# Optimization experiments

Measured on AMD Instinct MI355X. Metric: run time of the kernel, lower is better.

The kernel has to match this reference:

```python
import jax, jax.numpy as jnp
import numpy as np

B, L, D, N, NL = 8, 32768, 64, 16, 4


def setup_inputs() -> dict:
    key = jax.random.key(0)
    ks = jax.random.split(key, 32)
    r = lambda i, shape, s=1.0: s * jax.random.normal(ks[i], shape, dtype=jnp.float32)
    return {
        "inputs": r(0, (B, L)),
        "w_init": r(1, (D, 1), 0.5), "b_init": r(2, (D,), 0.1),
        "s4_ln_w": 1.0 + r(3, (NL, D), 0.05), "s4_ln_b": r(4, (NL, D), 0.05),
        "log_dt": r(5, (NL, D), 0.5) - 4.0,          # dt ~ exp(-4) ~ 0.018
        "log_A_real": r(6, (NL, D, N), 0.3),
        "A_imag": r(7, (NL, D, N)),
        "C_re": r(8, (NL, D, N), 0.5), "C_im": r(9, (NL, D, N), 0.5),
        "D_skip": r(10, (NL, D)),
        "s4_out_w": r(11, (NL, 2 * D, D), 0.1), "s4_out_b": r(12, (NL, 2 * D), 0.05),
        "ff_ln_w": 1.0 + r(13, (NL, D), 0.05), "ff_ln_b": r(14, (NL, D), 0.05),
        "ff_w1": r(15, (NL, 2 * D, D), 0.1), "ff_b1": r(16, (NL, 2 * D), 0.05),
        "ff_w2": r(17, (NL, D, 2 * D), 0.1), "ff_b2": r(18, (NL, D), 0.05),
        "norm_w": 1.0 + r(19, (D,), 0.05), "norm_b": r(20, (D,), 0.05),
        "w_final1": r(21, (D, D), 0.1), "b_final1": r(22, (D,), 0.05),
        "w_zero": r(23, (1, D), 0.02), "b_zero": r(24, (1,), 0.01),
    }


def _ln(x, w, b):
    # layernorm over channel dim of [B, D, L] (TransposedLN)
    m = jnp.mean(x, axis=1, keepdims=True)
    v = jnp.var(x, axis=1, keepdims=True)
    return (x - m) * jax.lax.rsqrt(v + 1e-5) * w[None, :, None] + b[None, :, None]


def _s4d(z, log_dt, log_A_real, A_imag, C_re, C_im, D_skip):
    # S4D (diagonal SSM) with ZOH discretization; z: [B, D, L]
    Lq = z.shape[-1]
    dt = jnp.exp(log_dt)                              # [D]
    A = -jnp.exp(log_A_real) + 1j * A_imag            # [D, N]
    dtA = A * dt[:, None]                             # [D, N]
    C = (C_re + 1j * C_im) * (jnp.exp(dtA) - 1.0) / A # dC = C * (e^{dtA}-1)/A
    t = jnp.arange(Lq)
    # Vandermonde kernel K[d, l] = 2 Re sum_n dC[d,n] e^{dtA[d,n] * l}
    K = 2.0 * jnp.real(jnp.einsum('dn,dnl->dl', C, jnp.exp(dtA[:, :, None] * t)))
    n = 2 * Lq
    y = jnp.fft.irfft(jnp.fft.rfft(z, n) * jnp.fft.rfft(K, n)[None], n)[..., :Lq]
    return y + D_skip[None, :, None] * z


def reference(inputs, w_init, b_init, s4_ln_w, s4_ln_b, log_dt, log_A_real,
              A_imag, C_re, C_im, D_skip, s4_out_w, s4_out_b, ff_ln_w, ff_ln_b,
              ff_w1, ff_b1, ff_w2, ff_b2, norm_w, norm_b, w_final1, b_final1,
              w_zero, b_zero):
    # init conv (1x1) + ReLU; inputs [B, L] -> x [B, D, L]
    x = jax.nn.relu(jnp.einsum('dc,bcl->bdl', w_init, inputs[:, None, :])
                    + b_init[None, :, None])
    for i in range(NL):
        # --- S4 residual block: LN -> S4D -> GELU -> 1x1 conv to 2D -> GLU ---
        z = _ln(x, s4_ln_w[i], s4_ln_b[i])
        y = _s4d(z, log_dt[i], log_A_real[i], A_imag[i], C_re[i], C_im[i], D_skip[i])
        y = jax.nn.gelu(y)
        u = jnp.einsum('ed,bdl->bel', s4_out_w[i], y) + s4_out_b[i][None, :, None]
        a, g = jnp.split(u, 2, axis=1)
        x = x + a * jax.nn.sigmoid(g)
        z = _ln(x, ff_ln_w[i], ff_ln_b[i])
        h = jax.nn.gelu(jnp.einsum('ed,bdl->bel', ff_w1[i], z) + ff_b1[i][None, :, None])
        x = x + jnp.einsum('de,bel->bdl', ff_w2[i], h) + ff_b2[i][None, :, None]
    # final norm + conv head
    x = _ln(x, norm_w, norm_b)
    x = jax.nn.relu(jnp.einsum('ed,bdl->bel', w_final1, x) + b_final1[None, :, None])
    x = jnp.einsum('od,bdl->bol', w_zero, x) + b_zero[None, :, None]
    return x[:, 0, :]  # squeeze out_channels=1 -> [B, L]
```

## Files before the change

### kernel.cpp

```cpp
#include <hip/hip_runtime.h>
#include <cmath>

constexpr int Bq = 8, Lq = 32768, Dq = 64, Nq = 16, NLq = 4;
constexpr int CLq = 128, NCq = 256;
constexpr int PT = Bq * Lq / 16;

typedef _Float16 f16;
typedef _Float16 half2t __attribute__((ext_vector_type(2)));
typedef _Float16 half4 __attribute__((ext_vector_type(4)));
typedef _Float16 half8 __attribute__((ext_vector_type(8)));
typedef float f32x4 __attribute__((ext_vector_type(4)));
typedef float f32x2 __attribute__((ext_vector_type(2)));

static __device__ __forceinline__ float sigm(float x) { return 1.0f / (1.0f + __expf(-x)); }
static __device__ __forceinline__ float gelu_t(float x) {
  return x * sigm(1.5957691216057308f * fmaf(0.044715f * x * x, x, x));
}

__global__ __launch_bounds__(128) void k_wtall(
    const float* __restrict__ log_dt, const float* __restrict__ log_A_real,
    const float* __restrict__ A_imag, const float* __restrict__ C_re,
    const float* __restrict__ C_im, const float* __restrict__ dskip,
    f32x2* __restrict__ LCL, half8* __restrict__ TF, half8* __restrict__ VF,
    half8* __restrict__ WF) {
  __shared__ f32x2 pw[129][16];
  __shared__ f32x2 lamS[16], dcS[16];
  __shared__ float Ks[128];
  int d = blockIdx.x & 63, L = blockIdx.x >> 6;
  half8* TFl = TF + (size_t)L * 131072;
  half8* VFl = VF + (size_t)L * 32768;
  half8* WFl = WF + (size_t)L * 32768;
  int t = threadIdx.x;
  if (t < 16) {
    int di = L * 64 + d;
    int idx = di * 16 + t;
    float dt = expf(log_dt[di]);
    float Ar = -expf(log_A_real[idx]);
    float Ai = A_imag[idx];
    float dr = Ar * dt, dmi = Ai * dt;
    float er = expf(dr);
    float lr = er * cosf(dmi), li = er * sinf(dmi);
    float inv = 1.0f / (Ar * Ar + Ai * Ai);
    float e1r = lr - 1.0f, e1i = li;
    float qr = (e1r * Ar + e1i * Ai) * inv;
    float qi = (e1i * Ar - e1r * Ai) * inv;
    float cr = C_re[idx], ci = C_im[idx];
    lamS[t] = f32x2{lr, li};
    dcS[t] = f32x2{2.0f * (cr * qr - ci * qi), 2.0f * (cr * qi + ci * qr)};
    float erc = expf(dr * 128.0f);
    f32x2 l128 = f32x2{erc * cosf(dmi * 128.0f), erc * sinf(dmi * 128.0f)};
    pw[128][t] = l128;
    LCL[(size_t)L * 1024 + d * 16 + t] = l128;
  }
  __syncthreads();
#pragma unroll
  for (int n = 0; n < 16; n++) {
    f32x2 lam = lamS[n];
    float pr = 1.f, pi = 0.f, br = lam.x, bi = lam.y;
    int e = t;
    while (e) {
      if (e & 1) { float tt = pr * br - pi * bi; pi = fmaf(pr, bi, pi * br); pr = tt; }
      float t2 = br * br - bi * bi; bi = 2.f * br * bi; br = t2; e >>= 1;
    }
    pw[t][n] = f32x2{pr, pi};
  }
  __syncthreads();
  {
    float k = 0.f;
#pragma unroll
    for (int n = 0; n < 16; n++) {
      f32x2 dc = dcS[n];
      f32x2 p = pw[t][n];
      k += dc.x * p.x - dc.y * p.y;
    }
    if (t == 0) k += dskip[L * 64 + d];
    Ks[t] = k;
  }
  __syncthreads();
  for (int s = t; s < 2048; s += 128) {
    int ln = s & 63, kt = (s >> 6) & 3, mt = s >> 8;
    int jo = mt * 16 + (ln & 15);
    int ji0 = kt * 32 + (ln >> 4) * 8;
    half8 v;
#pragma unroll
    for (int jj = 0; jj < 8; jj++) {
      int ji = ji0 + jj;
      v[jj] = (jo >= ji) ? (f16)Ks[jo - ji] : (f16)0.f;
    }
    TFl[(size_t)d * 2048 + s] = v;
  }
  for (int s = t; s < 512; s += 128) {
    int ln = s & 63, mt = s >> 6;
    int jo = mt * 16 + (ln & 15);
    int q0 = (ln >> 4) * 8;
    half8 v;
#pragma unroll
    for (int jj = 0; jj < 8; jj++) {
      int q = q0 + jj, n = q >> 1;
      f32x2 dc = dcS[n];
      f32x2 p = pw[jo + 1][n];
      float wr = dc.x * p.x - dc.y * p.y;
      float wi = dc.x * p.y + dc.y * p.x;
      v[jj] = (q & 1) ? (f16)(-wi) : (f16)wr;
    }
    VFl[(size_t)d * 512 + s] = v;
  }
  for (int s = t; s < 512; s += 128) {
    int ln = s & 63, kt = (s >> 6) & 3, nt = s >> 8;
    int p_ = nt * 16 + (ln & 15);
    int n = p_ >> 1;
    int j0 = kt * 32 + (ln >> 4) * 8;
    half8 v;
#pragma unroll
    for (int jj = 0; jj < 8; jj++) {
      f32x2 p = pw[127 - (j0 + jj)][n];
      v[jj] = (p_ & 1) ? (f16)p.y : (f16)p.x;
    }
    WFl[(size_t)d * 512 + s] = v;
  }
}

__global__ __launch_bounds__(512) void k_init3(
    const float* __restrict__ inp, const float* __restrict__ w_init,
    const float* __restrict__ b_init, const float* __restrict__ lnw,
    const float* __restrict__ lnb, float* __restrict__ X, f16* __restrict__ Z16) {
  __shared__ __align__(16) f16 ztile[64 * 132];
  int tid = threadIdx.x;
  int widx = tid >> 6, lane = tid & 63;
  int pl = lane & 15, qh = lane >> 4;
  for (int k = 0; k < 4; ++k) {
    int pt = blockIdx.x * 8 + widx + k * 4096;
    int pos = pt * 16 + pl;
    float v = inp[pos];
    float s = 0.f, s2 = 0.f;
    f32x4 o[4];
#pragma unroll
    for (int q = 0; q < 4; q++) {
      int d0 = q * 16 + qh * 4;
      f32x4 w4 = *(const f32x4*)(w_init + d0);
      f32x4 b4 = *(const f32x4*)(b_init + d0);
#pragma unroll
      for (int j = 0; j < 4; j++) {
        float t = fmaf(w4[j], v, b4[j]);
        t = t > 0.f ? t : 0.f;
        o[q][j] = t; s += t; s2 += t * t;
      }
      *(f32x4*)(X + (size_t)pos * 64 + d0) = o[q];
    }
    s += __shfl_xor(s, 16); s += __shfl_xor(s, 32);
    s2 += __shfl_xor(s2, 16); s2 += __shfl_xor(s2, 32);
    float m = s * (1.0f / 64.0f);
    float rstd = rsqrtf(s2 * (1.0f / 64.0f) - m * m + 1e-5f);
    int prow = widx * 16 + pl;
#pragma unroll
    for (int q = 0; q < 4; q++) {
      int d0 = q * 16 + qh * 4;
      f32x4 lw = *(const f32x4*)(lnw + d0);
      f32x4 lb = *(const f32x4*)(lnb + d0);
#pragma unroll
      for (int r = 0; r < 4; r++)
        ztile[(d0 + r) * 132 + prow] = (f16)fmaf((o[q][r] - m) * rstd, lw[r], lb[r]);
    }
    __syncthreads();
    {
      int d = tid >> 3, c0 = (tid & 7) * 16;
      half8 z0 = *(const half8*)(ztile + d * 132 + c0);
      half8 z1 = *(const half8*)(ztile + d * 132 + c0 + 8);
      size_t zoff = (size_t)d * 262144 + (size_t)(blockIdx.x * 8 + k * 4096) * 16;
      *(half8*)(Z16 + zoff + c0) = z0;
      *(half8*)(Z16 + zoff + c0 + 8) = z1;
    }
    __syncthreads();
  }
}

__global__ __launch_bounds__(256) void k_p1g(
    const f16* __restrict__ Z16, const half8* __restrict__ WF, f16* __restrict__ S16) {
  int tid = threadIdx.x;
  int lane = tid & 63;
  int task = blockIdx.x * 4 + (tid >> 6);
  int d = task >> 7, bct = task & 127;
  int bc0 = bct * 16;
  int pl = lane & 15, qh = lane >> 4;
  half8 az[4];
  const f16* zp = Z16 + ((size_t)d * 2048 + bc0 + pl) * 128 + qh * 8;
#pragma unroll
  for (int kt = 0; kt < 4; kt++) az[kt] = *(const half8*)(zp + kt * 32);
#pragma unroll
  for (int nt = 0; nt < 2; nt++) {
    f32x4 acc = f32x4{0.f, 0.f, 0.f, 0.f};
#pragma unroll
    for (int kt = 0; kt < 4; kt++)
      acc = __builtin_amdgcn_mfma_f32_16x16x32_f16(az[kt], WF[(size_t)d * 512 + (nt * 4 + kt) * 64 + lane], acc, 0, 0, 0);
#pragma unroll
    for (int r = 0; r < 4; r++)
      S16[((size_t)d * 2048 + bc0 + qh * 4 + r) * 32 + nt * 16 + pl] = (f16)acc[r];
  }
}

__global__ __launch_bounds__(128) void k_pass2(
    const f16* __restrict__ S16, const f32x2* __restrict__ LCLl, f16* __restrict__ Sc) {
  int d = blockIdx.x;
  int t = threadIdx.x;
  int n = t & 15, b = t >> 4;
  f32x2 lam = LCLl[d * 16 + n];
  float cr = 0.f, ci = 0.f;
  size_t base = ((size_t)d * 2048 + b * 256) * 32 + 2 * n;
  const f16* sp = S16 + base;
  f16* cp = Sc + base;
#pragma unroll 8
  for (int c = 0; c < 256; c++) {
    *(half2t*)(cp + (size_t)c * 32) = half2t{(f16)cr, (f16)ci};
    half2t v = *(const half2t*)(sp + (size_t)c * 32);
    float nr = fmaf(lam.x, cr, fmaf(-lam.y, ci, (float)v[0]));
    float ni = fmaf(lam.x, ci, fmaf(lam.y, cr, (float)v[1]));
    cr = nr; ci = ni;
  }
}

__global__ __launch_bounds__(256) void k_p3g2(
    const f16* __restrict__ Z16, const f16* __restrict__ Sc,
    const half8* __restrict__ TF, const half8* __restrict__ VF,
    f16* __restrict__ Y16) {
  int tid = threadIdx.x;
  int lane = tid & 63, widx = tid >> 6;
  int bct = blockIdx.x & 127, dg = blockIdx.x >> 7;
  int bc0 = bct * 16;
  int dbase = dg * 16 + widx * 4;
  int pl = lane & 15, qh = lane >> 4;
  half8 zb[4][4];
  half8 sb[4];
#pragma unroll
  for (int di = 0; di < 4; di++) {
    int d = dbase + di;
    const f16* zp = Z16 + ((size_t)d * 2048 + bc0 + pl) * 128 + qh * 8;
#pragma unroll
    for (int kt = 0; kt < 4; kt++) zb[di][kt] = *(const half8*)(zp + kt * 32);
    sb[di] = *(const half8*)(Sc + ((size_t)d * 2048 + bc0 + pl) * 32 + qh * 8);
  }
#pragma unroll
  for (int mt = 0; mt < 8; mt++) {
    const int KTM = mt / 2 + 1;
    f32x4 acc[4];
#pragma unroll
    for (int di = 0; di < 4; di++) {
      int d = dbase + di;
      acc[di] = f32x4{0.f, 0.f, 0.f, 0.f};
      const half8* tfp = TF + ((size_t)d * 8 + mt) * 256 + lane;
#pragma unroll
      for (int kt = 0; kt < KTM; kt++)
        acc[di] = __builtin_amdgcn_mfma_f32_16x16x32_f16(tfp[kt * 64], zb[di][kt], acc[di], 0, 0, 0);
      acc[di] = __builtin_amdgcn_mfma_f32_16x16x32_f16(VF[((size_t)d * 8 + mt) * 64 + lane], sb[di], acc[di], 0, 0, 0);
    }
#pragma unroll
    for (int r = 0; r < 4; r++) {
      int pos = (bc0 + pl) * 128 + mt * 16 + qh * 4 + r;
      half4 pk = half4{(f16)gelu_t(acc[0][r]), (f16)gelu_t(acc[1][r]),
                       (f16)gelu_t(acc[2][r]), (f16)gelu_t(acc[3][r])};
      *(half4*)(Y16 + (size_t)pos * 64 + dbase) = pk;
    }
  }
}

template <int WZ>
__global__ __launch_bounds__(512) void k_gluff3(
    const f16* __restrict__ Y16, const float* __restrict__ Wg, const float* __restrict__ bg,
    const float* __restrict__ W1, const float* __restrict__ b1,
    const float* __restrict__ W2, const float* __restrict__ b2,
    const float* __restrict__ lnw, const float* __restrict__ lnb,
    const float* __restrict__ nlnw, const float* __restrict__ nlnb,
    float* __restrict__ X, f16* __restrict__ Z16,
    const float* __restrict__ Wf, const float* __restrict__ bfb,
    const float* __restrict__ wz, const float* __restrict__ bz,
    float* __restrict__ outp) {
  __shared__ __align__(16) char smem[68352];
  int tid = threadIdx.x;
#pragma unroll
  for (int it = 0; it < 2; it++) {
    int s = it * 512 + tid;
    int l = s & 63, ks = (s >> 6) & 1, et = s >> 7;
    const float* wp = Wg + (et * 16 + (l & 15)) * 64 + ks * 32 + (l >> 4) * 8;
    f32x4 w0 = *(const f32x4*)wp, w1 = *(const f32x4*)(wp + 4);
    *(half8*)(smem + s * 16) = half8{(f16)w0[0], (f16)w0[1], (f16)w0[2], (f16)w0[3],
                                     (f16)w1[0], (f16)w1[1], (f16)w1[2], (f16)w1[3]};
  }
#pragma unroll
  for (int it = 0; it < 2; it++) {
    int s = it * 512 + tid;
    int l = s & 63, ks = (s >> 6) & 1, et = s >> 7;
    int pls = l & 15, qhs = l >> 4;
    const float* wp = W1 + (et * 16 + pls) * 64 + ks * 32 + qhs * 4;
    f32x4 w0 = *(const f32x4*)wp;
    f32x4 w1 = *(const f32x4*)(wp + 16);
    *(half8*)(smem + 16384 + s * 16) = half8{(f16)w0[0], (f16)w0[1], (f16)w0[2], (f16)w0[3],
                                             (f16)w1[0], (f16)w1[1], (f16)w1[2], (f16)w1[3]};
  }
#pragma unroll
  for (int it = 0; it < 2; it++) {
    int s = it * 512 + tid;
    int l = s & 63, ks = (s >> 6) & 3, dt = s >> 8;
    int pls = l & 15, qhs = l >> 4;
    const float* wp = W2 + (dt * 16 + pls) * 128 + ks * 32 + qhs * 4;
    f32x4 w0 = *(const f32x4*)wp;
    f32x4 w1 = *(const f32x4*)(wp + 16);
    *(half8*)(smem + 32768 + s * 16) = half8{(f16)w0[0], (f16)w0[1], (f16)w0[2], (f16)w0[3],
                                             (f16)w1[0], (f16)w1[1], (f16)w1[2], (f16)w1[3]};
  }
  for (int idx = tid; idx < 576; idx += 512) {
    float v;
    if (idx < 128) v = bg[idx];
    else if (idx < 256) v = b1[idx - 128];
    else if (idx < 320) v = b2[idx - 256];
    else if (idx < 384) v = lnw[idx - 320];
    else if (idx < 448) v = lnb[idx - 384];
    else if (idx < 512) v = nlnw[idx - 448];
    else v = nlnb[idx - 512];
    ((float*)(smem + 49152))[idx] = v;
  }
  if constexpr (!WZ) {
    if (tid < 512) {
      int s = tid;
      int l = s & 63, ks = (s >> 6) & 1, et = s >> 7;
      int pls = l & 15, qhs = l >> 4;
      const float* wp = Wf + (et * 16 + pls) * 64 + ks * 32 + qhs * 4;
      f32x4 w0 = *(const f32x4*)wp;
      f32x4 w1 = *(const f32x4*)(wp + 16);
      *(half8*)(smem + 51456 + s * 16) = half8{(f16)w0[0], (f16)w0[1], (f16)w0[2], (f16)w0[3],
                                               (f16)w1[0], (f16)w1[1], (f16)w1[2], (f16)w1[3]};
    }
    if (tid < 129) {
      float v = tid < 64 ? bfb[tid] : (tid < 128 ? wz[tid - 64] : bz[0]);
      ((float*)(smem + 59648))[tid] = v;
    }
  }
  __syncthreads();
  int lane = tid & 63, pl = lane & 15, qh = lane >> 4;
  int widx = tid >> 6;
  f16* ztile = (f16*)(smem + 51456);

  int pos = (blockIdx.x * 8 + widx) * 16 + pl;
  half8 yb0 = *(const half8*)(Y16 + (size_t)pos * 64 + qh * 8);
  half8 yb1 = *(const half8*)(Y16 + (size_t)pos * 64 + 32 + qh * 8);
  f32x4 xv[4];
#pragma unroll
  for (int q = 0; q < 4; q++) xv[q] = *(const f32x4*)(X + (size_t)pos * 64 + q * 16 + qh * 4);

  for (int k = 0; k < 4; ++k) {
    half8 nyb0{}, nyb1{};
    f32x4 nxv[4] = {};
    int npos = pos + 65536;
    if (k < 3) {
      nyb0 = *(const half8*)(Y16 + (size_t)npos * 64 + qh * 8);
      nyb1 = *(const half8*)(Y16 + (size_t)npos * 64 + 32 + qh * 8);
#pragma unroll
      for (int q = 0; q < 4; q++) nxv[q] = *(const f32x4*)(X + (size_t)npos * 64 + q * 16 + qh * 4);
    }

    unsigned sb = 0;
    asm volatile("" : "+v"(sb));
    const char* sm = smem + sb;
    const half8* sWg = (const half8*)sm;
    const half8* sW1 = (const half8*)(sm + 16384);
    const half8* sW2 = (const half8*)(sm + 32768);
    const float* sf = (const float*)(sm + 49152);
    f32x4 accg[8];
#pragma unroll
    for (int et = 0; et < 8; et++) accg[et] = *(const f32x4*)(sf + et * 16 + qh * 4);
#pragma unroll
    for (int et = 0; et < 8; et++)
      accg[et] = __builtin_amdgcn_mfma_f32_16x16x32_f16(sWg[(et * 2) * 64 + lane], yb0, accg[et], 0, 0, 0);
#pragma unroll
    for (int et = 0; et < 8; et++)
      accg[et] = __builtin_amdgcn_mfma_f32_16x16x32_f16(sWg[(et * 2 + 1) * 64 + lane], yb1, accg[et], 0, 0, 0);
    float s = 0.f, s2 = 0.f;
#pragma unroll
    for (int q = 0; q < 4; q++)
#pragma unroll
      for (int r = 0; r < 4; r++) {
        xv[q][r] += accg[q][r] * sigm(accg[q + 4][r]);
        s += xv[q][r]; s2 += xv[q][r] * xv[q][r];
      }
    s += __shfl_xor(s, 16); s += __shfl_xor(s, 32);
    s2 += __shfl_xor(s2, 16); s2 += __shfl_xor(s2, 32);
    float m = s * (1.0f / 64.0f);
    float rstd = rsqrtf(s2 * (1.0f / 64.0f) - m * m + 1e-5f);
    half4 zb4[4];
#pragma unroll
    for (int ks = 0; ks < 4; ks++) {
      f32x4 lw = *(const f32x4*)(sf + 320 + ks * 16 + qh * 4);
      f32x4 lb = *(const f32x4*)(sf + 384 + ks * 16 + qh * 4);
      half4 z;
#pragma unroll
      for (int r = 0; r < 4; r++) z[r] = (f16)fmaf((xv[ks][r] - m) * rstd, lw[r], lb[r]);
      zb4[ks] = z;
    }
    f32x4 acc1[8];
#pragma unroll
    for (int et = 0; et < 8; et++) acc1[et] = *(const f32x4*)(sf + 128 + et * 16 + qh * 4);
#pragma unroll
    for (int ks = 0; ks < 2; ks++) {
      half4 a = zb4[ks * 2], b = zb4[ks * 2 + 1];
      half8 zb8 = half8{a[0], a[1], a[2], a[3], b[0], b[1], b[2], b[3]};
#pragma unroll
      for (int et = 0; et < 8; et++)
        acc1[et] = __builtin_amdgcn_mfma_f32_16x16x32_f16(sW1[(et * 2 + ks) * 64 + lane], zb8, acc1[et], 0, 0, 0);
    }
    half4 h4[8];
#pragma unroll
    for (int et = 0; et < 8; et++)
      h4[et] = half4{(f16)gelu_t(acc1[et][0]), (f16)gelu_t(acc1[et][1]),
                     (f16)gelu_t(acc1[et][2]), (f16)gelu_t(acc1[et][3])};
    f32x4 acc2[4];
#pragma unroll
    for (int dt = 0; dt < 4; dt++) acc2[dt] = *(const f32x4*)(sf + 256 + dt * 16 + qh * 4);
#pragma unroll
    for (int ks = 0; ks < 4; ks++) {
      half4 a = h4[ks * 2], b = h4[ks * 2 + 1];
      half8 hb8 = half8{a[0], a[1], a[2], a[3], b[0], b[1], b[2], b[3]};
#pragma unroll
      for (int dt = 0; dt < 4; dt++)
        acc2[dt] = __builtin_amdgcn_mfma_f32_16x16x32_f16(sW2[(dt * 4 + ks) * 64 + lane], hb8, acc2[dt], 0, 0, 0);
    }
    s = 0.f; s2 = 0.f;
#pragma unroll
    for (int dt = 0; dt < 4; dt++) {
#pragma unroll
      for (int r = 0; r < 4; r++) {
        xv[dt][r] += acc2[dt][r];
        s += xv[dt][r]; s2 += xv[dt][r] * xv[dt][r];
      }
      if constexpr (WZ) *(f32x4*)(X + (size_t)pos * 64 + dt * 16 + qh * 4) = xv[dt];
    }
    s += __shfl_xor(s, 16); s += __shfl_xor(s, 32);
    s2 += __shfl_xor(s2, 16); s2 += __shfl_xor(s2, 32);
    float m2 = s * (1.0f / 64.0f);
    float rstd2 = rsqrtf(s2 * (1.0f / 64.0f) - m2 * m2 + 1e-5f);

    if constexpr (WZ) {
      int prow = widx * 16 + pl;
#pragma unroll
      for (int q = 0; q < 4; q++) {
        int d0 = q * 16 + qh * 4;
        f32x4 lw = *(const f32x4*)(sf + 448 + d0);
        f32x4 lb = *(const f32x4*)(sf + 512 + d0);
#pragma unroll
        for (int r = 0; r < 4; r++)
          ztile[(d0 + r) * 132 + prow] = (f16)fmaf((xv[q][r] - m2) * rstd2, lw[r], lb[r]);
      }
      __syncthreads();
      {
        int d = tid >> 3, c0 = (tid & 7) * 16;
        half8 z0 = *(const half8*)(ztile + d * 132 + c0);
        half8 z1 = *(const half8*)(ztile + d * 132 + c0 + 8);
        size_t zoff = (size_t)d * 262144 + (size_t)(blockIdx.x * 8 + k * 4096) * 16;
        *(half8*)(Z16 + zoff + c0) = z0;
        *(half8*)(Z16 + zoff + c0 + 8) = z1;
      }
      __syncthreads();
    } else {
      const half8* sWf = (const half8*)(sm + 51456);
      const float* hf = (const float*)(sm + 59648);
      half4 hz[4];
#pragma unroll
      for (int ks = 0; ks < 4; ks++) {
        f32x4 lw = *(const f32x4*)(sf + 448 + ks * 16 + qh * 4);
        f32x4 lb = *(const f32x4*)(sf + 512 + ks * 16 + qh * 4);
        half4 z;
#pragma unroll
        for (int r = 0; r < 4; r++) z[r] = (f16)fmaf((xv[ks][r] - m2) * rstd2, lw[r], lb[r]);
        hz[ks] = z;
      }
      f32x4 acch[4];
#pragma unroll
      for (int et = 0; et < 4; et++) acch[et] = *(const f32x4*)(hf + et * 16 + qh * 4);
#pragma unroll
      for (int ks = 0; ks < 2; ks++) {
        half4 a = hz[ks * 2], b = hz[ks * 2 + 1];
        half8 zb8 = half8{a[0], a[1], a[2], a[3], b[0], b[1], b[2], b[3]};
#pragma unroll
        for (int et = 0; et < 4; et++)
          acch[et] = __builtin_amdgcn_mfma_f32_16x16x32_f16(sWf[(et * 2 + ks) * 64 + lane], zb8, acch[et], 0, 0, 0);
      }
      float o = 0.f;
#pragma unroll
      for (int et = 0; et < 4; et++) {
        f32x4 wzv = *(const f32x4*)(hf + 64 + et * 16 + qh * 4);
#pragma unroll
        for (int r = 0; r < 4; r++) {
          float rv = acch[et][r];
          rv = rv > 0.f ? rv : 0.f;
          o = fmaf(wzv[r], rv, o);
        }
      }
      o += __shfl_xor(o, 16); o += __shfl_xor(o, 32);
      if (qh == 0) outp[pos] = o + hf[128];
    }

    if (k < 3) {
      yb0 = nyb0; yb1 = nyb1;
#pragma unroll
      for (int q = 0; q < 4; q++) xv[q] = nxv[q];
      pos = npos;
    }
  }
}

extern "C" void kernel_launch(void* const* d_in, const int* in_sizes, int n_in,
                              void* d_out, int out_size, void* d_ws, size_t ws_size,
                              hipStream_t stream) {
  (void)in_sizes; (void)n_in; (void)out_size; (void)ws_size;
  const float* inputs   = (const float*)d_in[0];
  const float* w_init   = (const float*)d_in[1];
  const float* b_init   = (const float*)d_in[2];
  const float* s4_ln_w  = (const float*)d_in[3];
  const float* s4_ln_b  = (const float*)d_in[4];
  const float* log_dt   = (const float*)d_in[5];
  const float* log_A    = (const float*)d_in[6];
  const float* A_imag   = (const float*)d_in[7];
  const float* C_re     = (const float*)d_in[8];
  const float* C_im     = (const float*)d_in[9];
  const float* D_skip   = (const float*)d_in[10];
  const float* s4_out_w = (const float*)d_in[11];
  const float* s4_out_b = (const float*)d_in[12];
  const float* ff_ln_w  = (const float*)d_in[13];
  const float* ff_ln_b  = (const float*)d_in[14];
  const float* ff_w1    = (const float*)d_in[15];
  const float* ff_b1    = (const float*)d_in[16];
  const float* ff_w2    = (const float*)d_in[17];
  const float* ff_b2    = (const float*)d_in[18];
  const float* norm_w   = (const float*)d_in[19];
  const float* norm_b   = (const float*)d_in[20];
  const float* w_final1 = (const float*)d_in[21];
  const float* b_final1 = (const float*)d_in[22];
  const float* w_zero   = (const float*)d_in[23];
  const float* b_zero   = (const float*)d_in[24];

  char* w8 = (char*)d_ws;
  size_t off = 0;
  float* X     = (float*)(w8 + off); off += (size_t)67108864;
  f16*   Z16   = (f16*)(w8 + off);   off += (size_t)33554432;
  f16*   Y16   = (f16*)(w8 + off);   off += (size_t)33554432;
  f16*   S16   = (f16*)(w8 + off);   off += (size_t)8388608;
  f16*   Sc    = (f16*)(w8 + off);   off += (size_t)8388608;
  f32x2* LCL   = (f32x2*)(w8 + off); off += 32768;
  half8* TF    = (half8*)(w8 + off); off += (size_t)8388608;
  half8* VF    = (half8*)(w8 + off); off += (size_t)2097152;
  half8* WF    = (half8*)(w8 + off); off += (size_t)2097152;

  k_wtall<<<256, 128, 0, stream>>>(log_dt, log_A, A_imag, C_re, C_im, D_skip,
                                   LCL, TF, VF, WF);
  k_init3<<<512, 512, 0, stream>>>(inputs, w_init, b_init, s4_ln_w, s4_ln_b, X, Z16);
  for (int i = 0; i < NLq; i++) {
    k_p1g<<<2048, 256, 0, stream>>>(Z16, WF + (size_t)i * 32768, S16);
    k_pass2<<<64, 128, 0, stream>>>(S16, LCL + i * 1024, Sc);
    k_p3g2<<<512, 256, 0, stream>>>(Z16, Sc, TF + (size_t)i * 131072, VF + (size_t)i * 32768, Y16);
    if (i < NLq - 1) {
      k_gluff3<1><<<512, 512, 0, stream>>>(Y16, s4_out_w + i * 8192, s4_out_b + i * 128,
                                           ff_w1 + i * 8192, ff_b1 + i * 128,
                                           ff_w2 + i * 8192, ff_b2 + i * 64,
                                           ff_ln_w + i * 64, ff_ln_b + i * 64,
                                           s4_ln_w + (i + 1) * 64, s4_ln_b + (i + 1) * 64,
                                           X, Z16, nullptr, nullptr, nullptr, nullptr, nullptr);
    } else {
      k_gluff3<0><<<512, 512, 0, stream>>>(Y16, s4_out_w + i * 8192, s4_out_b + i * 128,
                                           ff_w1 + i * 8192, ff_b1 + i * 128,
                                           ff_w2 + i * 8192, ff_b2 + i * 64,
                                           ff_ln_w + i * 64, ff_ln_b + i * 64,
                                           norm_w, norm_b,
                                           X, Z16, w_final1, b_final1, w_zero, b_zero,
                                           (float*)d_out);
    }
  }
}
```

Before: 532.2 us.

## Parallelize chunk-state scan with two-level blocked recurrence and drop gluff prefetch

```diff
diff --git a/kernel.cpp b/kernel.cpp
--- a/kernel.cpp
+++ b/kernel.cpp
@@ -21,8 +21,8 @@
     const float* __restrict__ log_dt, const float* __restrict__ log_A_real,
     const float* __restrict__ A_imag, const float* __restrict__ C_re,
     const float* __restrict__ C_im, const float* __restrict__ dskip,
-    f32x2* __restrict__ LCL, half8* __restrict__ TF, half8* __restrict__ VF,
-    half8* __restrict__ WF) {
+    f32x2* __restrict__ LCL, f32x2* __restrict__ LC2K, half8* __restrict__ TF,
+    half8* __restrict__ VF, half8* __restrict__ WF) {
   __shared__ f32x2 pw[129][16];
   __shared__ f32x2 lamS[16], dcS[16];
   __shared__ float Ks[128];
@@ -51,6 +51,13 @@
     f32x2 l128 = f32x2{erc * cosf(dmi * 128.0f), erc * sinf(dmi * 128.0f)};
     pw[128][t] = l128;
     LCL[(size_t)L * 1024 + d * 16 + t] = l128;
+    float br = l128.x, bi = l128.y;
+#pragma unroll
+    for (int q = 0; q < 4; q++) {
+      float t2 = br * br - bi * bi;
+      bi = 2.f * br * bi; br = t2;
+    }
+    LC2K[(size_t)L * 1024 + d * 16 + t] = f32x2{br, bi};
   }
   __syncthreads();
 #pragma unroll
@@ -198,23 +205,44 @@
   }
 }
 
-__global__ __launch_bounds__(128) void k_pass2(
-    const f16* __restrict__ S16, const f32x2* __restrict__ LCLl, f16* __restrict__ Sc) {
-  int d = blockIdx.x;
+__global__ __launch_bounds__(256) void k_pass2(
+    const f16* __restrict__ S16, const f32x2* __restrict__ LCLl,
+    const f32x2* __restrict__ LC2Kl, f16* __restrict__ Sc) {
+  __shared__ f32x2 gc[16][17];
+  int blk = blockIdx.x;
+  int d = blk >> 3, b = blk & 7;
   int t = threadIdx.x;
-  int n = t & 15, b = t >> 4;
+  int n = t & 15, g = t >> 4;
   f32x2 lam = LCLl[d * 16 + n];
+  size_t base = ((size_t)d * 2048 + b * 256 + g * 16) * 32 + 2 * n;
+  const f16* sp = S16 + base;
   float cr = 0.f, ci = 0.f;
-  size_t base = ((size_t)d * 2048 + b * 256) * 32 + 2 * n;
-  const f16* sp = S16 + base;
-  f16* cp = Sc + base;
-#pragma unroll 8
-  for (int c = 0; c < 256; c++) {
-    *(half2t*)(cp + (size_t)c * 32) = half2t{(f16)cr, (f16)ci};
-    half2t v = *(const half2t*)(sp + (size_t)c * 32);
+#pragma unroll 4
+  for (int j = 0; j < 16; j++) {
+    half2t v = *(const half2t*)(sp + (size_t)j * 32);
     float nr = fmaf(lam.x, cr, fmaf(-lam.y, ci, (float)v[0]));
     float ni = fmaf(lam.x, ci, fmaf(lam.y, cr, (float)v[1]));
     cr = nr; ci = ni;
+  }
+  gc[g][n] = f32x2{cr, ci};
+  __syncthreads();
+  f32x2 l2 = LC2Kl[d * 16 + n];
+  float er = 0.f, ei = 0.f;
+  for (int gg = 0; gg < g; gg++) {
+    f32x2 c = gc[gg][n];
+    float nr = fmaf(l2.x, er, fmaf(-l2.y, ei, c.x));
+    float ni = fmaf(l2.x, ei, fmaf(l2.y, er, c.y));
+    er = nr; ei = ni;
+  }
+  f16* cp = Sc + base;
+  float cr2 = er, ci2 = ei;
+#pragma unroll 4
+  for (int j = 0; j < 16; j++) {
+    *(half2t*)(cp + (size_t)j * 32) = half2t{(f16)cr2, (f16)ci2};
+    half2t v = *(const half2t*)(sp + (size_t)j * 32);
+    float nr = fmaf(lam.x, cr2, fmaf(-lam.y, ci2, (float)v[0]));
+    float ni = fmaf(lam.x, ci2, fmaf(lam.y, cr2, (float)v[1]));
+    cr2 = nr; ci2 = ni;
   }
 }
 
@@ -338,23 +366,14 @@
   int widx = tid >> 6;
   f16* ztile = (f16*)(smem + 51456);
 
-  int pos = (blockIdx.x * 8 + widx) * 16 + pl;
-  half8 yb0 = *(const half8*)(Y16 + (size_t)pos * 64 + qh * 8);
-  half8 yb1 = *(const half8*)(Y16 + (size_t)pos * 64 + 32 + qh * 8);
-  f32x4 xv[4];
-#pragma unroll
-  for (int q = 0; q < 4; q++) xv[q] = *(const f32x4*)(X + (size_t)pos * 64 + q * 16 + qh * 4);
-
   for (int k = 0; k < 4; ++k) {
-    half8 nyb0{}, nyb1{};
-    f32x4 nxv[4] = {};
-    int npos = pos + 65536;
-    if (k < 3) {
-      nyb0 = *(const half8*)(Y16 + (size_t)npos * 64 + qh * 8);
-      nyb1 = *(const half8*)(Y16 + (size_t)npos * 64 + 32 + qh * 8);
-#pragma unroll
-      for (int q = 0; q < 4; q++) nxv[q] = *(const f32x4*)(X + (size_t)npos * 64 + q * 16 + qh * 4);
-    }
+    int pt = blockIdx.x * 8 + widx + k * 4096;
+    int pos = pt * 16 + pl;
+    half8 yb0 = *(const half8*)(Y16 + (size_t)pos * 64 + qh * 8);
+    half8 yb1 = *(const half8*)(Y16 + (size_t)pos * 64 + 32 + qh * 8);
+    f32x4 xv[4];
+#pragma unroll
+    for (int q = 0; q < 4; q++) xv[q] = *(const f32x4*)(X + (size_t)pos * 64 + q * 16 + qh * 4);
 
     unsigned sb = 0;
     asm volatile("" : "+v"(sb));
@@ -494,13 +513,6 @@
       }
       o += __shfl_xor(o, 16); o += __shfl_xor(o, 32);
       if (qh == 0) outp[pos] = o + hf[128];
-    }
-
-    if (k < 3) {
-      yb0 = nyb0; yb1 = nyb1;
-#pragma unroll
-      for (int q = 0; q < 4; q++) xv[q] = nxv[q];
-      pos = npos;
     }
   }
 }
@@ -543,16 +555,17 @@
   f16*   S16   = (f16*)(w8 + off);   off += (size_t)8388608;
   f16*   Sc    = (f16*)(w8 + off);   off += (size_t)8388608;
   f32x2* LCL   = (f32x2*)(w8 + off); off += 32768;
+  f32x2* LC2K  = (f32x2*)(w8 + off); off += 32768;
   half8* TF    = (half8*)(w8 + off); off += (size_t)8388608;
   half8* VF    = (half8*)(w8 + off); off += (size_t)2097152;
   half8* WF    = (half8*)(w8 + off); off += (size_t)2097152;
 
   k_wtall<<<256, 128, 0, stream>>>(log_dt, log_A, A_imag, C_re, C_im, D_skip,
-                                   LCL, TF, VF, WF);
+                                   LCL, LC2K, TF, VF, WF);
   k_init3<<<512, 512, 0, stream>>>(inputs, w_init, b_init, s4_ln_w, s4_ln_b, X, Z16);
   for (int i = 0; i < NLq; i++) {
     k_p1g<<<2048, 256, 0, stream>>>(Z16, WF + (size_t)i * 32768, S16);
-    k_pass2<<<64, 128, 0, stream>>>(S16, LCL + i * 1024, Sc);
+    k_pass2<<<512, 256, 0, stream>>>(S16, LCL + i * 1024, LC2K + i * 1024, Sc);
     k_p3g2<<<512, 256, 0, stream>>>(Z16, Sc, TF + (size_t)i * 131072, VF + (size_t)i * 32768, Y16);
     if (i < NLq - 1) {
       k_gluff3<1><<<512, 512, 0, stream>>>(Y16, s4_out_w + i * 8192, s4_out_b + i * 128,
```

Measured after the change: 469.7 us. 1.13x faster.
